# Kernel tuning notes

Hardware: AMD Instinct MI355X
Metric: run time of the kernel (lower is better)

Reference implementation:

```python
import jax, jax.numpy as jnp
import numpy as np

NC = 4
X = Y = Z = 64
IMG_SHAPE = (96, 96, 96)
SPAN = 2          # FILTER_SIZE = [5,5,5]
NUM_ITER = 4
DIL = 2           # DILATION = 2.0
SMOOTH_DISTANCE_INIT = 0.3
PRIOR_DISTANCE_INIT = 0.3


def _ind(d):
    # mirrors _get_ind from the torch code
    return (d, 0) if d > 0 else (0, -d)


def _sl(a, b):
    # slice(a, -b) with -0 -> None, mirrors _negative
    return slice(a, -b if b else None)


def _offsets():
    for dx in range(-SPAN, SPAN + 1):
        for dy in range(-SPAN, SPAN + 1):
            for dz in range(-SPAN, SPAN + 1):
                yield dx, dy, dz


def _lin_resize_axis(x, axis, out):
    # 1D linear interpolation matching torch align_corners=True
    n = x.shape[axis]
    if out == n:
        return x
    pos = jnp.arange(out, dtype=x.dtype) * ((n - 1) / (out - 1))
    i0 = jnp.clip(jnp.floor(pos).astype(jnp.int32), 0, n - 1)
    i1 = jnp.clip(i0 + 1, 0, n - 1)
    w = pos - i0.astype(x.dtype)
    shp = [1] * x.ndim
    shp[axis] = out
    w = w.reshape(shp)
    return jnp.take(x, i0, axis=axis) * (1 - w) + jnp.take(x, i1, axis=axis) * w


def _resize3d(x, out_sz):
    # trilinear, align_corners=True, separable over the 3 spatial axes of [b,c,X,Y,Z]
    for ax, o in zip((2, 3, 4), out_sz):
        x = _lin_resize_axis(x, ax, o)
    return x


def _smooth_gaussian(feats):
    # feats: [b, c, X, Y, Z] -> gaussian [b, 5,5,5, X, Y, Z]
    b = feats.shape[0]
    sp = feats.shape[2:]
    g = jnp.zeros((b, 5, 5, 5) + sp, feats.dtype)
    for dx, dy, dz in _offsets():
        dx1, dx2 = _ind(dx); dy1, dy2 = _ind(dy); dz1, dz2 = _ind(dz)
        a = feats[:, :, _sl(dx1, dx2), _sl(dy1, dy2), _sl(dz1, dz2)]
        c = feats[:, :, _sl(dx2, dx1), _sl(dy2, dy1), _sl(dz2, dz1)]
        e = jnp.exp(-0.5 * jnp.sum((a - c) ** 2, axis=1))
        g = g.at[:, dx + SPAN, dy + SPAN, dz + SPAN,
                 _sl(dx2, dx1), _sl(dy2, dy1), _sl(dz2, dz1)].set(e)
    return g


def _prior_gaussian(f1, f2):
    # f1, f2: [b, c, x, y, z] (already downsampled) -> [b, 5,5,5, x, y, z]
    b = f1.shape[0]
    sp = f1.shape[2:]
    g = jnp.zeros((b, 5, 5, 5) + sp, f1.dtype)
    for dx, dy, dz in _offsets():
        dx1, dx2 = _ind(dx); dy1, dy2 = _ind(dy); dz1, dz2 = _ind(dz)
        a = f1[:, :, _sl(dx2, dx1), _sl(dy2, dy1), _sl(dz2, dz1)]
        c = f2[:, :, _sl(dx1, dx2), _sl(dy1, dy2), _sl(dz1, dz2)]
        e = jnp.exp(-0.5 * jnp.sum((a - c) ** 2, axis=1))
        g = g.at[:, dx + SPAN, dy + SPAN, dz + SPAN,
                 _sl(dx2, dx1), _sl(dy2, dy1), _sl(dz2, dz1)].set(e)
    return g


def _message(p, g):
    # p: [b, nc, x, y, z]; g: [b, 5,5,5, x, y, z]
    out = jnp.zeros_like(p)
    for dx, dy, dz in _offsets():
        dx1, dx2 = _ind(dx); dy1, dy2 = _ind(dy); dz1, dz2 = _ind(dz)
        a = p[:, :, _sl(dx1, dx2), _sl(dy1, dy2), _sl(dz1, dz2)]
        w = g[:, None, dx + SPAN, dy + SPAN, dz + SPAN,
              _sl(dx2, dx1), _sl(dy2, dy1), _sl(dz2, dz1)]
        out = out.at[:, :, _sl(dx2, dx1), _sl(dy2, dy1), _sl(dz2, dz1)].add(a * w)
    return out


def setup_inputs() -> dict:
    key = jax.random.key(0)
    ks = jax.random.split(key, 6)
    unary = jax.random.normal(ks[0], (1, NC, X, Y, Z), jnp.float32)
    img = jax.random.normal(ks[1], (1, 2, X, Y, Z), jnp.float32)
    atlas = jax.random.normal(ks[2], (1, 2, X, Y, Z), jnp.float32)
    atlas_label = jax.random.uniform(ks[3], (1, X, Y, Z, NC), jnp.float32)
    patch_start = jax.random.randint(ks[4], (1, 3), 0, 32, jnp.int32)
    return {
        "unary": unary,
        "img": img,
        "atlas": atlas,
        "atlas_label": atlas_label,
        "patch_start": patch_start,
        "smooth_norm": jnp.array([1.0 / SMOOTH_DISTANCE_INIT], jnp.float32),
        "smooth_weight": jnp.ones((NC,), jnp.float32),
        "prior_norm": jnp.array([1.0 / PRIOR_DISTANCE_INIT], jnp.float32),
        "prior_weight": jnp.ones(IMG_SHAPE, jnp.float32),
        "compat_w": jnp.eye(NC, dtype=jnp.float32),
    }


def reference(unary, img, atlas, atlas_label, patch_start,
              smooth_norm, smooth_weight, prior_norm, prior_weight, compat_w):
    b, nc, x, y, z = unary.shape
    ds = (x // DIL, y // DIL, z // DIL)  # floor(in*0.5) == ceil(in/2) for even dims

    # similarity kernels
    sg = _smooth_gaussian(img * smooth_norm)                      # [b,5,5,5,x,y,z]
    f1 = _resize3d(img * prior_norm, ds)
    f2 = _resize3d(atlas * prior_norm, ds)
    pg = _prior_gaussian(f1, f2)                                  # [b,5,5,5,x/2,y/2,z/2]

    # prior message is independent of q_values: compute once
    al = jnp.transpose(atlas_label, (0, 4, 1, 2, 3))              # [b,nc,x,y,z]
    al_ds = _resize3d(al, ds)
    pm = _resize3d(_message(al_ds, pg), (x, y, z))                # [b,nc,x,y,z]
    pw = jax.lax.dynamic_slice(
        prior_weight,
        (patch_start[0, 0], patch_start[0, 1], patch_start[0, 2]),
        (x, y, z))
    prior_term = pw[None, None] * pm

    q = unary
    for _ in range(NUM_ITER):
        p = jax.nn.softmax(q, axis=1)
        sm = _message(p, sg)
        pred = smooth_weight[None, :, None, None, None] * sm + prior_term
        q = unary + jnp.einsum('oc,bcxyz->boxyz', compat_w, pred)  # 1x1x1 compat conv
    return q
```

## Files before the change

kernel.cpp:

```cpp
#include <hip/hip_runtime.h>

#define NN 64
#define N3 (64*64*64)
#define DS 32
#define DS3 (32*32*32)

#define LOG2E 1.4426950408889634f
#define FSCALE 0.8493218002880191f

typedef _Float16 h2  __attribute__((ext_vector_type(2)));
typedef __fp16   h2f __attribute__((ext_vector_type(2)));

__device__ __forceinline__ float fexp2(float x) { return __builtin_amdgcn_exp2f(x); }

__device__ __forceinline__ h2 u2h(unsigned u) { union { unsigned u; h2 h; } c; c.u = u; return c.h; }
__device__ __forceinline__ unsigned h2u(h2 h) { union { unsigned u; h2 h; } c; c.h = h; return c.u; }
__device__ __forceinline__ h2 pkh(float a, float b) {
    union { h2f a; h2 b; } c; c.a = __builtin_amdgcn_cvt_pkrtz(a, b); return c.b;
}
__device__ __forceinline__ float fdot2(h2 a, h2 b) {
    union { h2 h; h2f f; } ca, cb; ca.h = a; cb.h = b;
    return __builtin_amdgcn_fdot2(ca.f, cb.f, 0.0f, false);
}

__device__ __forceinline__ void axw(int j, float scale, int nmax, int& i0, int& i1, float& w) {
    float pos = (float)j * scale;
    int f = (int)floorf(pos);
    if (f < 0) f = 0;
    if (f > nmax) f = nmax;
    i0 = f;
    i1 = (f + 1 <= nmax) ? f + 1 : nmax;
    w = pos - (float)f;
}


__global__ __launch_bounds__(128) void k_downsample(
    const float* __restrict__ img, const float* __restrict__ atlas,
    const float* __restrict__ alabel, const float* __restrict__ pnorm,
    unsigned* __restrict__ f1pk, uint4* __restrict__ nb)
{
    int idx = blockIdx.x * 128 + threadIdx.x;
    int z = idx & 31, y = (idx >> 5) & 31, x = idx >> 10;

    const float scale = 63.0f / 31.0f;
    int x0,x1,y0,y1,z0,z1; float wx,wy,wz;
    axw(x, scale, 63, x0, x1, wx);
    axw(y, scale, 63, y0, y1, wy);
    axw(z, scale, 63, z0, z1, wz);

    float w000=(1-wx)*(1-wy)*(1-wz), w001=(1-wx)*(1-wy)*wz;
    float w010=(1-wx)*wy*(1-wz),     w011=(1-wx)*wy*wz;
    float w100=wx*(1-wy)*(1-wz),     w101=wx*(1-wy)*wz;
    float w110=wx*wy*(1-wz),         w111=wx*wy*wz;

    int c000=(x0*NN+y0)*NN+z0, c001=(x0*NN+y0)*NN+z1;
    int c010=(x0*NN+y1)*NN+z0, c011=(x0*NN+y1)*NN+z1;
    int c100=(x1*NN+y0)*NN+z0, c101=(x1*NN+y0)*NN+z1;
    int c110=(x1*NN+y1)*NN+z0, c111=(x1*NN+y1)*NN+z1;

    auto tri = [&](const float* p) -> float {
        return p[c000]*w000 + p[c001]*w001 + p[c010]*w010 + p[c011]*w011
             + p[c100]*w100 + p[c101]*w101 + p[c110]*w110 + p[c111]*w111;
    };
    float pnf = pnorm[0] * FSCALE;
    f1pk[idx] = h2u(pkh(pnf*tri(img), pnf*tri(img + N3)));

    auto tril = [&](int c) -> float {
        return alabel[c000*4+c]*w000 + alabel[c001*4+c]*w001 + alabel[c010*4+c]*w010 + alabel[c011*4+c]*w011
             + alabel[c100*4+c]*w100 + alabel[c101*4+c]*w101 + alabel[c110*4+c]*w110 + alabel[c111*4+c]*w111;
    };
    nb[idx] = make_uint4(h2u(pkh(pnf*tri(atlas), pnf*tri(atlas + N3))),
                         h2u(pkh(tril(0), tril(1))),
                         h2u(pkh(tril(2), tril(3))), 0u);
}

__global__ __launch_bounds__(128) void k_prior_msg(
    const unsigned* __restrict__ f1pk, const uint4* __restrict__ nb,
    float4* __restrict__ pm)
{
    int idx = blockIdx.x * 128 + threadIdx.x;
    int z = idx & 31, y = (idx >> 5) & 31, x = idx >> 10;

    h2 ncf = -u2h(f1pk[idx]);
    float a0=0.f, a1=0.f, a2=0.f, a3=0.f;
    for (int dx = -2; dx <= 2; ++dx) {
        int xx = x + dx; if ((unsigned)xx >= DS) continue;
        for (int dy = -2; dy <= 2; ++dy) {
            int yy = y + dy; if ((unsigned)yy >= DS) continue;
            int base = (xx*DS + yy)*DS;
            #pragma unroll
            for (int dz = -2; dz <= 2; ++dz) {
                int zz = z + dz; if ((unsigned)zz >= DS) continue;
                uint4 v = nb[base + zz];
                h2 d = u2h(v.x) + ncf;
                float t = fdot2(d, d);
                float w = fexp2(-t);
                h2 l01 = u2h(v.y), l23 = u2h(v.z);
                a0 += w*(float)l01.x; a1 += w*(float)l01.y;
                a2 += w*(float)l23.x; a3 += w*(float)l23.y;
            }
        }
    }
    pm[idx] = make_float4(a0, a1, a2, a3);
}


#define TXD 8
#define TYD 8
#define TZR 8
#define RZ 2
#define TZD (TZR*RZ)
#define HX 12
#define HY 12
#define HZ 20
#define PZ 22

template<bool QV_IN, bool QV_OUT>
__global__ __launch_bounds__(1024, 4) void k_iter(
    const float* __restrict__ qin,
    const float* __restrict__ unary,
    const float* __restrict__ img,
    const float* __restrict__ snorm,
    const float* __restrict__ sweight,
    const float* __restrict__ compat,
    const float4* __restrict__ pm,
    const float* __restrict__ pweight,
    const int* __restrict__ pstart,
    float* __restrict__ qout)
{
    __shared__ __align__(16) uint2    pS[HX][HY][PZ];
    __shared__ __align__(8)  unsigned fS[HX][HY][PZ];
    __shared__ __align__(16) float4   accS[TXD*TYD*TZR][2];

    const int tzg = threadIdx.x, ty = threadIdx.y;
    const int tx = threadIdx.z & 7, s = threadIdx.z >> 3;
    const int x0b = blockIdx.z * TXD, y0b = blockIdx.y * TYD, z0b = blockIdx.x * TZD;
    const int tid = threadIdx.x + TZR*threadIdx.y + TZR*TYD*threadIdx.z;
    const float sc = snorm[0] * FSCALE;

    #pragma unroll
    for (int rr = 0; rr < 3; ++rr) {
        int i = tid + rr*1024;
        if (i < HX*HY*HZ) {
            int lz = i % HZ; int r = i / HZ;
            int ly = r % HY; int lx = r / HY;
            int gx = x0b + lx - 2, gy = y0b + ly - 2, gz = z0b + lz - 2;
            uint2 pu = make_uint2(0u, 0u);
            unsigned fu = 0u;
            if ((unsigned)gx < NN && (unsigned)gy < NN && (unsigned)gz < NN) {
                int g = (gx*NN + gy)*NN + gz;
                float q0, q1, q2, q3;
                if (QV_IN) {
                    float4 qv = reinterpret_cast<const float4*>(qin)[g];
                    q0 = qv.x; q1 = qv.y; q2 = qv.z; q3 = qv.w;
                } else {
                    q0 = qin[g]; q1 = qin[g+N3]; q2 = qin[g+2*N3]; q3 = qin[g+3*N3];
                }
                float m = fmaxf(fmaxf(q0,q1), fmaxf(q2,q3));
                float e0 = fexp2((q0-m)*LOG2E);
                float e1 = fexp2((q1-m)*LOG2E);
                float e2 = fexp2((q2-m)*LOG2E);
                float e3 = fexp2((q3-m)*LOG2E);
                float inv = 1.0f/(e0+e1+e2+e3);
                pu = make_uint2(h2u(pkh(e0*inv, e1*inv)), h2u(pkh(e2*inv, e3*inv)));
                fu = h2u(pkh(img[g]*sc, img[g+N3]*sc));
            }
            pS[lx][ly][lz] = pu;
            fS[lx][ly][lz] = fu;
        }
    }

    const int tz0 = tzg * RZ;
    const int gx = x0b + tx, gy = y0b + ty, gz = z0b + tz0;

    float4 pr0 = make_float4(0.f,0.f,0.f,0.f), pr1 = make_float4(0.f,0.f,0.f,0.f);
    if (s == 1) {
        const float S13 = 31.0f / 63.0f;
        float posx = (float)gx * S13; int xc0 = (int)posx; float wxf = posx - (float)xc0;
        int xc1 = xc0 < 31 ? xc0+1 : 31;
        float posy = (float)gy * S13; int yc0 = (int)posy; float wyf = posy - (float)yc0;
        int yc1 = yc0 < 31 ? yc0+1 : 31;
        int r00i = (xc0*DS+yc0)*DS, r01i = (xc0*DS+yc1)*DS;
        int r10i = (xc1*DS+yc0)*DS, r11i = (xc1*DS+yc1)*DS;
        auto upz = [&](int gzv) -> float4 {
            float posz = (float)gzv * S13; int zc0 = (int)posz; float wzf = posz - (float)zc0;
            int zc1 = zc0 < 31 ? zc0+1 : 31;
            float4 p000 = pm[r00i+zc0], p001 = pm[r00i+zc1];
            float4 p010 = pm[r01i+zc0], p011 = pm[r01i+zc1];
            float4 p100 = pm[r10i+zc0], p101 = pm[r10i+zc1];
            float4 p110 = pm[r11i+zc0], p111 = pm[r11i+zc1];
            float w000=(1-wxf)*(1-wyf)*(1-wzf), w001=(1-wxf)*(1-wyf)*wzf;
            float w010=(1-wxf)*wyf*(1-wzf),     w011=(1-wxf)*wyf*wzf;
            float w100=wxf*(1-wyf)*(1-wzf),     w101=wxf*(1-wyf)*wzf;
            float w110=wxf*wyf*(1-wzf),         w111=wxf*wyf*wzf;
            float4 r;
            r.x = w000*p000.x + w001*p001.x + w010*p010.x + w011*p011.x + w100*p100.x + w101*p101.x + w110*p110.x + w111*p111.x;
            r.y = w000*p000.y + w001*p001.y + w010*p010.y + w011*p011.y + w100*p100.y + w101*p101.y + w110*p110.y + w111*p111.y;
            r.z = w000*p000.z + w001*p001.z + w010*p010.z + w011*p011.z + w100*p100.z + w101*p101.z + w110*p110.z + w111*p111.z;
            r.w = w000*p000.w + w001*p001.w + w010*p010.w + w011*p011.w + w100*p100.w + w101*p101.w + w110*p110.w + w111*p111.w;
            return r;
        };
        pr0 = upz(gz);
        pr1 = upz(gz+1);
        int ps0 = pstart[0], ps1 = pstart[1], ps2 = pstart[2];
        int pwbase = (ps0+gx)*96*96 + (ps1+gy)*96 + ps2 + gz;
        float pwa = pweight[pwbase], pwb = pweight[pwbase+1];
        pr0.x *= pwa; pr0.y *= pwa; pr0.z *= pwa; pr0.w *= pwa;
        pr1.x *= pwb; pr1.y *= pwb; pr1.z *= pwb; pr1.w *= pwb;
    }

    __syncthreads();

    h2 ncf0 = -u2h(fS[tx+2][ty+2][tz0+2]);
    h2 ncf1 = -u2h(fS[tx+2][ty+2][tz0+3]);

    float4 acc0 = make_float4(0.f,0.f,0.f,0.f);
    float4 acc1 = make_float4(0.f,0.f,0.f,0.f);

    for (int p = s; p < 25; p += 2) {
        int dx = p / 5, dy = p - dx*5;
        const uint4* pp = reinterpret_cast<const uint4*>(&pS[tx+dx][ty+dy][tz0]);
        const uint2* fp = reinterpret_cast<const uint2*>(&fS[tx+dx][ty+dy][tz0]);
        uint4 qa = pp[0], qb = pp[1], qc = pp[2];
        uint2 fa = fp[0], fb = fp[1], fc = fp[2];

        unsigned fz[6]  = { fa.x, fa.y, fb.x, fb.y, fc.x, fc.y };
        unsigned p01[6] = { qa.x, qa.z, qb.x, qb.z, qc.x, qc.z };
        unsigned p23[6] = { qa.y, qa.w, qb.y, qb.w, qc.y, qc.w };

        #pragma unroll
        for (int dz = 0; dz < 5; ++dz) {
            {
                h2 d = u2h(fz[dz]) + ncf0;
                float t = fdot2(d, d);
                float w = fexp2(-t);
                h2 a = u2h(p01[dz]), b = u2h(p23[dz]);
                acc0.x += w*(float)a.x; acc0.y += w*(float)a.y;
                acc0.z += w*(float)b.x; acc0.w += w*(float)b.y;
            }
            {
                h2 d = u2h(fz[dz+1]) + ncf1;
                float t = fdot2(d, d);
                float w = fexp2(-t);
                h2 a = u2h(p01[dz+1]), b = u2h(p23[dz+1]);
                acc1.x += w*(float)a.x; acc1.y += w*(float)a.y;
                acc1.z += w*(float)b.x; acc1.w += w*(float)b.y;
            }
        }
    }

    const int pid = (tx*TYD + ty)*TZR + tzg;
    if (s == 0) {
        accS[pid][0] = acc0;
        accS[pid][1] = acc1;
    }
    __syncthreads();

    if (s == 1) {
        float4 o0 = accS[pid][0], o1 = accS[pid][1];
        acc0.x += o0.x; acc0.y += o0.y; acc0.z += o0.z; acc0.w += o0.w;
        acc1.x += o1.x; acc1.y += o1.y; acc1.z += o1.z; acc1.w += o1.w;

        const int g = (gx*NN + gy)*NN + gz;
        float2 un0 = *(const float2*)(unary + 0*N3 + g);
        float2 un1 = *(const float2*)(unary + 1*N3 + g);
        float2 un2 = *(const float2*)(unary + 2*N3 + g);
        float2 un3 = *(const float2*)(unary + 3*N3 + g);
        float sw0 = sweight[0], sw1 = sweight[1], sw2 = sweight[2], sw3 = sweight[3];
        float cw[16];
        #pragma unroll
        for (int k = 0; k < 16; ++k) cw[k] = compat[k];

        float p0, p1, p2, p3;
        float r00, r10, r20, r30, r01, r11, r21, r31;
        p0 = sw0*acc0.x + pr0.x; p1 = sw1*acc0.y + pr0.y; p2 = sw2*acc0.z + pr0.z; p3 = sw3*acc0.w + pr0.w;
        r00 = un0.x + cw[0]*p0  + cw[1]*p1  + cw[2]*p2  + cw[3]*p3;
        r10 = un1.x + cw[4]*p0  + cw[5]*p1  + cw[6]*p2  + cw[7]*p3;
        r20 = un2.x + cw[8]*p0  + cw[9]*p1  + cw[10]*p2 + cw[11]*p3;
        r30 = un3.x + cw[12]*p0 + cw[13]*p1 + cw[14]*p2 + cw[15]*p3;
        p0 = sw0*acc1.x + pr1.x; p1 = sw1*acc1.y + pr1.y; p2 = sw2*acc1.z + pr1.z; p3 = sw3*acc1.w + pr1.w;
        r01 = un0.y + cw[0]*p0  + cw[1]*p1  + cw[2]*p2  + cw[3]*p3;
        r11 = un1.y + cw[4]*p0  + cw[5]*p1  + cw[6]*p2  + cw[7]*p3;
        r21 = un2.y + cw[8]*p0  + cw[9]*p1  + cw[10]*p2 + cw[11]*p3;
        r31 = un3.y + cw[12]*p0 + cw[13]*p1 + cw[14]*p2 + cw[15]*p3;

        if (QV_OUT) {
            reinterpret_cast<float4*>(qout)[g]   = make_float4(r00, r10, r20, r30);
            reinterpret_cast<float4*>(qout)[g+1] = make_float4(r01, r11, r21, r31);
        } else {
            *(float2*)(qout + 0*N3 + g) = make_float2(r00, r01);
            *(float2*)(qout + 1*N3 + g) = make_float2(r10, r11);
            *(float2*)(qout + 2*N3 + g) = make_float2(r20, r21);
            *(float2*)(qout + 3*N3 + g) = make_float2(r30, r31);
        }
    }
}


extern "C" void kernel_launch(void* const* d_in, const int* in_sizes, int n_in,
                              void* d_out, int out_size, void* d_ws, size_t ws_size,
                              hipStream_t stream)
{
    const float* unary   = (const float*)d_in[0];
    const float* img     = (const float*)d_in[1];
    const float* atlas   = (const float*)d_in[2];
    const float* alabel  = (const float*)d_in[3];
    const int*   pstart  = (const int*)d_in[4];
    const float* snorm   = (const float*)d_in[5];
    const float* sweight = (const float*)d_in[6];
    const float* pnorm   = (const float*)d_in[7];
    const float* pweight = (const float*)d_in[8];
    const float* compat  = (const float*)d_in[9];
    float* out = (float*)d_out;
    float* ws  = (float*)d_ws;

    float*    qA   = ws;
    float*    qB   = ws + 4*N3;
    unsigned* f1pk = (unsigned*)(ws + 8*N3);
    uint4*    nbuf = (uint4*)(f1pk + DS3);
    float4*   pm   = (float4*)(nbuf + DS3);

    k_downsample<<<DS3/128, 128, 0, stream>>>(img, atlas, alabel, pnorm, f1pk, nbuf);
    k_prior_msg<<<DS3/128, 128, 0, stream>>>(f1pk, nbuf, pm);

    dim3 grid(NN/TZD, NN/TYD, NN/TXD), block(TZR, TYD, 16);
    k_iter<false,true><<<grid, block, 0, stream>>>(unary, unary, img, snorm, sweight, compat, pm, pweight, pstart, qA);
    k_iter<true, true><<<grid, block, 0, stream>>>(qA,    unary, img, snorm, sweight, compat, pm, pweight, pstart, qB);
    k_iter<true, true><<<grid, block, 0, stream>>>(qB,    unary, img, snorm, sweight, compat, pm, pweight, pstart, qA);
    k_iter<true,false><<<grid, block, 0, stream>>>(qA,    unary, img, snorm, sweight, compat, pm, pweight, pstart, out);
}
```

Measured before the change: 95.58 us.

## Fuse four mean-field iterations into one cooperative kernel with grid sync

Replaces four separate per-iteration launches with a single cooperative launch that loops over the iterations and uses grid-wide syncs between them. The image feature tile, the prior upsample term and the centre features are loaded once and kept in shared memory and registers across iterations, removing launch gaps and repeated loads. The message accumulation also moves from fp32 scalar FMAs to packed fp16 FMAs, which cuts instruction count but lowers accumulation precision. Grid sync needs every block resident at once (the grid is 256 blocks of 1024 threads) and adds its own barrier cost.

```diff
diff --git a/kernel.cpp b/kernel.cpp
--- a/kernel.cpp
+++ b/kernel.cpp
@@ -1,4 +1,7 @@
 #include <hip/hip_runtime.h>
+#include <hip/hip_cooperative_groups.h>
+
+namespace cg = cooperative_groups;
 
 #define NN 64
 #define N3 (64*64*64)
@@ -115,9 +118,7 @@
 #define HZ 20
 #define PZ 22
 
-template<bool QV_IN, bool QV_OUT>
-__global__ __launch_bounds__(1024, 4) void k_iter(
-    const float* __restrict__ qin,
+__global__ __launch_bounds__(1024) void k_coop(
     const float* __restrict__ unary,
     const float* __restrict__ img,
     const float* __restrict__ snorm,
@@ -126,11 +127,15 @@
     const float4* __restrict__ pm,
     const float* __restrict__ pweight,
     const int* __restrict__ pstart,
-    float* __restrict__ qout)
+    float* __restrict__ qA,
+    float* __restrict__ qB,
+    float* __restrict__ out)
 {
     __shared__ __align__(16) uint2    pS[HX][HY][PZ];
     __shared__ __align__(8)  unsigned fS[HX][HY][PZ];
-    __shared__ __align__(16) float4   accS[TXD*TYD*TZR][2];
+    __shared__ __align__(16) uint2    accS[TXD*TYD*TZR][2];
+
+    cg::grid_group gridg = cg::this_grid();
 
     const int tzg = threadIdx.x, ty = threadIdx.y;
     const int tx = threadIdx.z & 7, s = threadIdx.z >> 3;
@@ -145,33 +150,19 @@
             int lz = i % HZ; int r = i / HZ;
             int ly = r % HY; int lx = r / HY;
             int gx = x0b + lx - 2, gy = y0b + ly - 2, gz = z0b + lz - 2;
-            uint2 pu = make_uint2(0u, 0u);
             unsigned fu = 0u;
             if ((unsigned)gx < NN && (unsigned)gy < NN && (unsigned)gz < NN) {
                 int g = (gx*NN + gy)*NN + gz;
-                float q0, q1, q2, q3;
-                if (QV_IN) {
-                    float4 qv = reinterpret_cast<const float4*>(qin)[g];
-                    q0 = qv.x; q1 = qv.y; q2 = qv.z; q3 = qv.w;
-                } else {
-                    q0 = qin[g]; q1 = qin[g+N3]; q2 = qin[g+2*N3]; q3 = qin[g+3*N3];
-                }
-                float m = fmaxf(fmaxf(q0,q1), fmaxf(q2,q3));
-                float e0 = fexp2((q0-m)*LOG2E);
-                float e1 = fexp2((q1-m)*LOG2E);
-                float e2 = fexp2((q2-m)*LOG2E);
-                float e3 = fexp2((q3-m)*LOG2E);
-                float inv = 1.0f/(e0+e1+e2+e3);
-                pu = make_uint2(h2u(pkh(e0*inv, e1*inv)), h2u(pkh(e2*inv, e3*inv)));
                 fu = h2u(pkh(img[g]*sc, img[g+N3]*sc));
             }
-            pS[lx][ly][lz] = pu;
             fS[lx][ly][lz] = fu;
         }
     }
 
     const int tz0 = tzg * RZ;
     const int gx = x0b + tx, gy = y0b + ty, gz = z0b + tz0;
+    const int g = (gx*NN + gy)*NN + gz;
+    const int pid = (tx*TYD + ty)*TZR + tzg;
 
     float4 pr0 = make_float4(0.f,0.f,0.f,0.f), pr1 = make_float4(0.f,0.f,0.f,0.f);
     if (s == 1) {
@@ -211,88 +202,124 @@
 
     __syncthreads();
 
-    h2 ncf0 = -u2h(fS[tx+2][ty+2][tz0+2]);
-    h2 ncf1 = -u2h(fS[tx+2][ty+2][tz0+3]);
-
-    float4 acc0 = make_float4(0.f,0.f,0.f,0.f);
-    float4 acc1 = make_float4(0.f,0.f,0.f,0.f);
-
-    for (int p = s; p < 25; p += 2) {
-        int dx = p / 5, dy = p - dx*5;
-        const uint4* pp = reinterpret_cast<const uint4*>(&pS[tx+dx][ty+dy][tz0]);
-        const uint2* fp = reinterpret_cast<const uint2*>(&fS[tx+dx][ty+dy][tz0]);
-        uint4 qa = pp[0], qb = pp[1], qc = pp[2];
-        uint2 fa = fp[0], fb = fp[1], fc = fp[2];
-
-        unsigned fz[6]  = { fa.x, fa.y, fb.x, fb.y, fc.x, fc.y };
-        unsigned p01[6] = { qa.x, qa.z, qb.x, qb.z, qc.x, qc.z };
-        unsigned p23[6] = { qa.y, qa.w, qb.y, qb.w, qc.y, qc.w };
+    const h2 ncf0 = -u2h(fS[tx+2][ty+2][tz0+2]);
+    const h2 ncf1 = -u2h(fS[tx+2][ty+2][tz0+3]);
+
+    for (int it = 0; it < 4; ++it) {
+        const float* qin  = (it == 0) ? unary : ((it == 2) ? qB : qA);
+        float*       qout = (it == 0) ? qA : ((it == 1) ? qB : ((it == 2) ? qA : out));
+        const bool vec_in  = (it != 0);
+        const bool vec_out = (it != 3);
 
         #pragma unroll
-        for (int dz = 0; dz < 5; ++dz) {
-            {
-                h2 d = u2h(fz[dz]) + ncf0;
-                float t = fdot2(d, d);
-                float w = fexp2(-t);
-                h2 a = u2h(p01[dz]), b = u2h(p23[dz]);
-                acc0.x += w*(float)a.x; acc0.y += w*(float)a.y;
-                acc0.z += w*(float)b.x; acc0.w += w*(float)b.y;
-            }
-            {
-                h2 d = u2h(fz[dz+1]) + ncf1;
-                float t = fdot2(d, d);
-                float w = fexp2(-t);
-                h2 a = u2h(p01[dz+1]), b = u2h(p23[dz+1]);
-                acc1.x += w*(float)a.x; acc1.y += w*(float)a.y;
-                acc1.z += w*(float)b.x; acc1.w += w*(float)b.y;
-            }
-        }
-    }
-
-    const int pid = (tx*TYD + ty)*TZR + tzg;
-    if (s == 0) {
-        accS[pid][0] = acc0;
-        accS[pid][1] = acc1;
-    }
-    __syncthreads();
-
-    if (s == 1) {
-        float4 o0 = accS[pid][0], o1 = accS[pid][1];
-        acc0.x += o0.x; acc0.y += o0.y; acc0.z += o0.z; acc0.w += o0.w;
-        acc1.x += o1.x; acc1.y += o1.y; acc1.z += o1.z; acc1.w += o1.w;
-
-        const int g = (gx*NN + gy)*NN + gz;
-        float2 un0 = *(const float2*)(unary + 0*N3 + g);
-        float2 un1 = *(const float2*)(unary + 1*N3 + g);
-        float2 un2 = *(const float2*)(unary + 2*N3 + g);
-        float2 un3 = *(const float2*)(unary + 3*N3 + g);
-        float sw0 = sweight[0], sw1 = sweight[1], sw2 = sweight[2], sw3 = sweight[3];
-        float cw[16];
-        #pragma unroll
-        for (int k = 0; k < 16; ++k) cw[k] = compat[k];
-
-        float p0, p1, p2, p3;
-        float r00, r10, r20, r30, r01, r11, r21, r31;
-        p0 = sw0*acc0.x + pr0.x; p1 = sw1*acc0.y + pr0.y; p2 = sw2*acc0.z + pr0.z; p3 = sw3*acc0.w + pr0.w;
-        r00 = un0.x + cw[0]*p0  + cw[1]*p1  + cw[2]*p2  + cw[3]*p3;
-        r10 = un1.x + cw[4]*p0  + cw[5]*p1  + cw[6]*p2  + cw[7]*p3;
-        r20 = un2.x + cw[8]*p0  + cw[9]*p1  + cw[10]*p2 + cw[11]*p3;
-        r30 = un3.x + cw[12]*p0 + cw[13]*p1 + cw[14]*p2 + cw[15]*p3;
-        p0 = sw0*acc1.x + pr1.x; p1 = sw1*acc1.y + pr1.y; p2 = sw2*acc1.z + pr1.z; p3 = sw3*acc1.w + pr1.w;
-        r01 = un0.y + cw[0]*p0  + cw[1]*p1  + cw[2]*p2  + cw[3]*p3;
-        r11 = un1.y + cw[4]*p0  + cw[5]*p1  + cw[6]*p2  + cw[7]*p3;
-        r21 = un2.y + cw[8]*p0  + cw[9]*p1  + cw[10]*p2 + cw[11]*p3;
-        r31 = un3.y + cw[12]*p0 + cw[13]*p1 + cw[14]*p2 + cw[15]*p3;
-
-        if (QV_OUT) {
-            reinterpret_cast<float4*>(qout)[g]   = make_float4(r00, r10, r20, r30);
-            reinterpret_cast<float4*>(qout)[g+1] = make_float4(r01, r11, r21, r31);
-        } else {
-            *(float2*)(qout + 0*N3 + g) = make_float2(r00, r01);
-            *(float2*)(qout + 1*N3 + g) = make_float2(r10, r11);
-            *(float2*)(qout + 2*N3 + g) = make_float2(r20, r21);
-            *(float2*)(qout + 3*N3 + g) = make_float2(r30, r31);
-        }
+        for (int rr = 0; rr < 3; ++rr) {
+            int i = tid + rr*1024;
+            if (i < HX*HY*HZ) {
+                int lz = i % HZ; int r = i / HZ;
+                int ly = r % HY; int lx = r / HY;
+                int ggx = x0b + lx - 2, ggy = y0b + ly - 2, ggz = z0b + lz - 2;
+                uint2 pu = make_uint2(0u, 0u);
+                if ((unsigned)ggx < NN && (unsigned)ggy < NN && (unsigned)ggz < NN) {
+                    int gg = (ggx*NN + ggy)*NN + ggz;
+                    float q0, q1, q2, q3;
+                    if (vec_in) {
+                        float4 qv = reinterpret_cast<const float4*>(qin)[gg];
+                        q0 = qv.x; q1 = qv.y; q2 = qv.z; q3 = qv.w;
+                    } else {
+                        q0 = qin[gg]; q1 = qin[gg+N3]; q2 = qin[gg+2*N3]; q3 = qin[gg+3*N3];
+                    }
+                    float m = fmaxf(fmaxf(q0,q1), fmaxf(q2,q3));
+                    float e0 = fexp2((q0-m)*LOG2E);
+                    float e1 = fexp2((q1-m)*LOG2E);
+                    float e2 = fexp2((q2-m)*LOG2E);
+                    float e3 = fexp2((q3-m)*LOG2E);
+                    float inv = 1.0f/(e0+e1+e2+e3);
+                    pu = make_uint2(h2u(pkh(e0*inv, e1*inv)), h2u(pkh(e2*inv, e3*inv)));
+                }
+                pS[lx][ly][lz] = pu;
+            }
+        }
+        __syncthreads();
+
+        h2 a01_0 = (h2)0, a23_0 = (h2)0, a01_1 = (h2)0, a23_1 = (h2)0;
+
+        for (int p = s; p < 25; p += 2) {
+            int dx = p / 5, dy = p - dx*5;
+            const uint4* pp = reinterpret_cast<const uint4*>(&pS[tx+dx][ty+dy][tz0]);
+            const uint2* fp = reinterpret_cast<const uint2*>(&fS[tx+dx][ty+dy][tz0]);
+            uint4 qa = pp[0], qb = pp[1], qc = pp[2];
+            uint2 fa = fp[0], fb = fp[1], fc = fp[2];
+
+            unsigned fz[6]  = { fa.x, fa.y, fb.x, fb.y, fc.x, fc.y };
+            unsigned p01[6] = { qa.x, qa.z, qb.x, qb.z, qc.x, qc.z };
+            unsigned p23[6] = { qa.y, qa.w, qb.y, qb.w, qc.y, qc.w };
+
+            #pragma unroll
+            for (int dz = 0; dz < 5; ++dz) {
+                {
+                    h2 d = u2h(fz[dz]) + ncf0;
+                    float w = fexp2(-fdot2(d, d));
+                    h2 w2 = pkh(w, w);
+                    a01_0 = w2 * u2h(p01[dz]) + a01_0;
+                    a23_0 = w2 * u2h(p23[dz]) + a23_0;
+                }
+                {
+                    h2 d = u2h(fz[dz+1]) + ncf1;
+                    float w = fexp2(-fdot2(d, d));
+                    h2 w2 = pkh(w, w);
+                    a01_1 = w2 * u2h(p01[dz+1]) + a01_1;
+                    a23_1 = w2 * u2h(p23[dz+1]) + a23_1;
+                }
+            }
+        }
+
+        if (s == 0) {
+            accS[pid][0] = make_uint2(h2u(a01_0), h2u(a23_0));
+            accS[pid][1] = make_uint2(h2u(a01_1), h2u(a23_1));
+        }
+        __syncthreads();
+
+        if (s == 1) {
+            uint2 o0 = accS[pid][0], o1 = accS[pid][1];
+            h2 t01_0 = a01_0 + u2h(o0.x), t23_0 = a23_0 + u2h(o0.y);
+            h2 t01_1 = a01_1 + u2h(o1.x), t23_1 = a23_1 + u2h(o1.y);
+
+            float2 un0 = *(const float2*)(unary + 0*N3 + g);
+            float2 un1 = *(const float2*)(unary + 1*N3 + g);
+            float2 un2 = *(const float2*)(unary + 2*N3 + g);
+            float2 un3 = *(const float2*)(unary + 3*N3 + g);
+            float sw0 = sweight[0], sw1 = sweight[1], sw2 = sweight[2], sw3 = sweight[3];
+            float cw[16];
+            #pragma unroll
+            for (int k = 0; k < 16; ++k) cw[k] = compat[k];
+
+            float p0, p1, p2, p3;
+            float r00, r10, r20, r30, r01, r11, r21, r31;
+            p0 = sw0*(float)t01_0.x + pr0.x; p1 = sw1*(float)t01_0.y + pr0.y;
+            p2 = sw2*(float)t23_0.x + pr0.z; p3 = sw3*(float)t23_0.y + pr0.w;
+            r00 = un0.x + cw[0]*p0  + cw[1]*p1  + cw[2]*p2  + cw[3]*p3;
+            r10 = un1.x + cw[4]*p0  + cw[5]*p1  + cw[6]*p2  + cw[7]*p3;
+            r20 = un2.x + cw[8]*p0  + cw[9]*p1  + cw[10]*p2 + cw[11]*p3;
+            r30 = un3.x + cw[12]*p0 + cw[13]*p1 + cw[14]*p2 + cw[15]*p3;
+            p0 = sw0*(float)t01_1.x + pr1.x; p1 = sw1*(float)t01_1.y + pr1.y;
+            p2 = sw2*(float)t23_1.x + pr1.z; p3 = sw3*(float)t23_1.y + pr1.w;
+            r01 = un0.y + cw[0]*p0  + cw[1]*p1  + cw[2]*p2  + cw[3]*p3;
+            r11 = un1.y + cw[4]*p0  + cw[5]*p1  + cw[6]*p2  + cw[7]*p3;
+            r21 = un2.y + cw[8]*p0  + cw[9]*p1  + cw[10]*p2 + cw[11]*p3;
+            r31 = un3.y + cw[12]*p0 + cw[13]*p1 + cw[14]*p2 + cw[15]*p3;
+
+            if (vec_out) {
+                reinterpret_cast<float4*>(qout)[g]   = make_float4(r00, r10, r20, r30);
+                reinterpret_cast<float4*>(qout)[g+1] = make_float4(r01, r11, r21, r31);
+            } else {
+                *(float2*)(qout + 0*N3 + g) = make_float2(r00, r01);
+                *(float2*)(qout + 1*N3 + g) = make_float2(r10, r11);
+                *(float2*)(qout + 2*N3 + g) = make_float2(r20, r21);
+                *(float2*)(qout + 3*N3 + g) = make_float2(r30, r31);
+            }
+        }
+
+        if (it != 3) gridg.sync();
     }
 }
 
@@ -324,8 +351,9 @@
     k_prior_msg<<<DS3/128, 128, 0, stream>>>(f1pk, nbuf, pm);
 
     dim3 grid(NN/TZD, NN/TYD, NN/TXD), block(TZR, TYD, 16);
-    k_iter<false,true><<<grid, block, 0, stream>>>(unary, unary, img, snorm, sweight, compat, pm, pweight, pstart, qA);
-    k_iter<true, true><<<grid, block, 0, stream>>>(qA,    unary, img, snorm, sweight, compat, pm, pweight, pstart, qB);
-    k_iter<true, true><<<grid, block, 0, stream>>>(qB,    unary, img, snorm, sweight, compat, pm, pweight, pstart, qA);
-    k_iter<true,false><<<grid, block, 0, stream>>>(qA,    unary, img, snorm, sweight, compat, pm, pweight, pstart, out);
-}
+    void* args[] = {
+        (void*)&unary, (void*)&img, (void*)&snorm, (void*)&sweight, (void*)&compat,
+        (void*)&pm, (void*)&pweight, (void*)&pstart, (void*)&qA, (void*)&qB, (void*)&out
+    };
+    hipLaunchCooperativeKernel((const void*)k_coop, grid, block, args, 0, stream);
+}
```

After: 204.2 us. 114% more time.

## Split stencil taps four ways per voxel with packed half accumulation

Applied to the files above, without the earlier changes.

The main iteration kernel now uses smaller z tiles (8 instead of 16) and splits the 25 dx/dy taps across four thread groups instead of two, so each block covers fewer voxels with more threads per voxel. Accumulation switches from fp32 scalar FMAs to packed fp16 FMAs, and partial sums are reduced through shared memory as packed halves. The prior-term upsample moves to the group that does the final reduction and overlaps with the stencil work. This raises parallelism and shortens the ALU chain, at the cost of a larger halo-to-interior ratio and lower fp16 accumulation precision.

```diff
diff --git a/kernel.cpp b/kernel.cpp
--- a/kernel.cpp
+++ b/kernel.cpp
@@ -107,16 +107,16 @@
 
 #define TXD 8
 #define TYD 8
-#define TZR 8
+#define TZD 8
+#define TZR 4
 #define RZ 2
-#define TZD (TZR*RZ)
 #define HX 12
 #define HY 12
-#define HZ 20
-#define PZ 22
+#define HZ 12
+#define PZ 14
 
 template<bool QV_IN, bool QV_OUT>
-__global__ __launch_bounds__(1024, 4) void k_iter(
+__global__ __launch_bounds__(1024, 8) void k_iter(
     const float* __restrict__ qin,
     const float* __restrict__ unary,
     const float* __restrict__ img,
@@ -130,16 +130,16 @@
 {
     __shared__ __align__(16) uint2    pS[HX][HY][PZ];
     __shared__ __align__(8)  unsigned fS[HX][HY][PZ];
-    __shared__ __align__(16) float4   accS[TXD*TYD*TZR][2];
+    __shared__ __align__(16) uint4    accS[3][TXD*TYD*TZR];
 
     const int tzg = threadIdx.x, ty = threadIdx.y;
     const int tx = threadIdx.z & 7, s = threadIdx.z >> 3;
     const int x0b = blockIdx.z * TXD, y0b = blockIdx.y * TYD, z0b = blockIdx.x * TZD;
-    const int tid = threadIdx.x + TZR*threadIdx.y + TZR*TYD*threadIdx.z;
+    const int tid = threadIdx.x + TZR*threadIdx.y + (TZR*TYD)*threadIdx.z;
     const float sc = snorm[0] * FSCALE;
 
     #pragma unroll
-    for (int rr = 0; rr < 3; ++rr) {
+    for (int rr = 0; rr < 2; ++rr) {
         int i = tid + rr*1024;
         if (i < HX*HY*HZ) {
             int lz = i % HZ; int r = i / HZ;
@@ -169,12 +169,57 @@
             fS[lx][ly][lz] = fu;
         }
     }
+    __syncthreads();
 
     const int tz0 = tzg * RZ;
     const int gx = x0b + tx, gy = y0b + ty, gz = z0b + tz0;
 
+    const h2 ncf0 = -u2h(fS[tx+2][ty+2][tz0+2]);
+    const h2 ncf1 = -u2h(fS[tx+2][ty+2][tz0+3]);
+
+    h2 a01_0 = (h2)0, a23_0 = (h2)0, a01_1 = (h2)0, a23_1 = (h2)0;
+
+    #pragma unroll
+    for (int pp = 0; pp < 7; ++pp) {
+        int p = (3 - s) + 4*pp;
+        if (p < 25) {
+            int dx = p / 5, dy = p - 5*dx;
+            const uint4* pv = reinterpret_cast<const uint4*>(&pS[tx+dx][ty+dy][tz0]);
+            const uint2* fv = reinterpret_cast<const uint2*>(&fS[tx+dx][ty+dy][tz0]);
+            uint4 qa = pv[0], qb = pv[1], qc = pv[2];
+            uint2 fa = fv[0], fb = fv[1], fc = fv[2];
+
+            unsigned fz[6]  = { fa.x, fa.y, fb.x, fb.y, fc.x, fc.y };
+            unsigned p01[6] = { qa.x, qa.z, qb.x, qb.z, qc.x, qc.z };
+            unsigned p23[6] = { qa.y, qa.w, qb.y, qb.w, qc.y, qc.w };
+
+            #pragma unroll
+            for (int dz = 0; dz < 5; ++dz) {
+                {
+                    h2 d = u2h(fz[dz]) + ncf0;
+                    float w = fexp2(-fdot2(d, d));
+                    h2 w2 = pkh(w, w);
+                    a01_0 = w2 * u2h(p01[dz]) + a01_0;
+                    a23_0 = w2 * u2h(p23[dz]) + a23_0;
+                }
+                {
+                    h2 d = u2h(fz[dz+1]) + ncf1;
+                    float w = fexp2(-fdot2(d, d));
+                    h2 w2 = pkh(w, w);
+                    a01_1 = w2 * u2h(p01[dz+1]) + a01_1;
+                    a23_1 = w2 * u2h(p23[dz+1]) + a23_1;
+                }
+            }
+        }
+    }
+
+    const int pid = (tx*TYD + ty)*TZR + tzg;
+    if (s != 0) {
+        accS[s-1][pid] = make_uint4(h2u(a01_0), h2u(a23_0), h2u(a01_1), h2u(a23_1));
+    }
+
     float4 pr0 = make_float4(0.f,0.f,0.f,0.f), pr1 = make_float4(0.f,0.f,0.f,0.f);
-    if (s == 1) {
+    if (s == 0) {
         const float S13 = 31.0f / 63.0f;
         float posx = (float)gx * S13; int xc0 = (int)posx; float wxf = posx - (float)xc0;
         int xc1 = xc0 < 31 ? xc0+1 : 31;
@@ -211,55 +256,13 @@
 
     __syncthreads();
 
-    h2 ncf0 = -u2h(fS[tx+2][ty+2][tz0+2]);
-    h2 ncf1 = -u2h(fS[tx+2][ty+2][tz0+3]);
-
-    float4 acc0 = make_float4(0.f,0.f,0.f,0.f);
-    float4 acc1 = make_float4(0.f,0.f,0.f,0.f);
-
-    for (int p = s; p < 25; p += 2) {
-        int dx = p / 5, dy = p - dx*5;
-        const uint4* pp = reinterpret_cast<const uint4*>(&pS[tx+dx][ty+dy][tz0]);
-        const uint2* fp = reinterpret_cast<const uint2*>(&fS[tx+dx][ty+dy][tz0]);
-        uint4 qa = pp[0], qb = pp[1], qc = pp[2];
-        uint2 fa = fp[0], fb = fp[1], fc = fp[2];
-
-        unsigned fz[6]  = { fa.x, fa.y, fb.x, fb.y, fc.x, fc.y };
-        unsigned p01[6] = { qa.x, qa.z, qb.x, qb.z, qc.x, qc.z };
-        unsigned p23[6] = { qa.y, qa.w, qb.y, qb.w, qc.y, qc.w };
-
+    if (s == 0) {
         #pragma unroll
-        for (int dz = 0; dz < 5; ++dz) {
-            {
-                h2 d = u2h(fz[dz]) + ncf0;
-                float t = fdot2(d, d);
-                float w = fexp2(-t);
-                h2 a = u2h(p01[dz]), b = u2h(p23[dz]);
-                acc0.x += w*(float)a.x; acc0.y += w*(float)a.y;
-                acc0.z += w*(float)b.x; acc0.w += w*(float)b.y;
-            }
-            {
-                h2 d = u2h(fz[dz+1]) + ncf1;
-                float t = fdot2(d, d);
-                float w = fexp2(-t);
-                h2 a = u2h(p01[dz+1]), b = u2h(p23[dz+1]);
-                acc1.x += w*(float)a.x; acc1.y += w*(float)a.y;
-                acc1.z += w*(float)b.x; acc1.w += w*(float)b.y;
-            }
-        }
-    }
-
-    const int pid = (tx*TYD + ty)*TZR + tzg;
-    if (s == 0) {
-        accS[pid][0] = acc0;
-        accS[pid][1] = acc1;
-    }
-    __syncthreads();
-
-    if (s == 1) {
-        float4 o0 = accS[pid][0], o1 = accS[pid][1];
-        acc0.x += o0.x; acc0.y += o0.y; acc0.z += o0.z; acc0.w += o0.w;
-        acc1.x += o1.x; acc1.y += o1.y; acc1.z += o1.z; acc1.w += o1.w;
+        for (int j = 0; j < 3; ++j) {
+            uint4 v = accS[j][pid];
+            a01_0 += u2h(v.x); a23_0 += u2h(v.y);
+            a01_1 += u2h(v.z); a23_1 += u2h(v.w);
+        }
 
         const int g = (gx*NN + gy)*NN + gz;
         float2 un0 = *(const float2*)(unary + 0*N3 + g);
@@ -273,12 +276,14 @@
 
         float p0, p1, p2, p3;
         float r00, r10, r20, r30, r01, r11, r21, r31;
-        p0 = sw0*acc0.x + pr0.x; p1 = sw1*acc0.y + pr0.y; p2 = sw2*acc0.z + pr0.z; p3 = sw3*acc0.w + pr0.w;
+        p0 = sw0*(float)a01_0.x + pr0.x; p1 = sw1*(float)a01_0.y + pr0.y;
+        p2 = sw2*(float)a23_0.x + pr0.z; p3 = sw3*(float)a23_0.y + pr0.w;
         r00 = un0.x + cw[0]*p0  + cw[1]*p1  + cw[2]*p2  + cw[3]*p3;
         r10 = un1.x + cw[4]*p0  + cw[5]*p1  + cw[6]*p2  + cw[7]*p3;
         r20 = un2.x + cw[8]*p0  + cw[9]*p1  + cw[10]*p2 + cw[11]*p3;
         r30 = un3.x + cw[12]*p0 + cw[13]*p1 + cw[14]*p2 + cw[15]*p3;
-        p0 = sw0*acc1.x + pr1.x; p1 = sw1*acc1.y + pr1.y; p2 = sw2*acc1.z + pr1.z; p3 = sw3*acc1.w + pr1.w;
+        p0 = sw0*(float)a01_1.x + pr1.x; p1 = sw1*(float)a01_1.y + pr1.y;
+        p2 = sw2*(float)a23_1.x + pr1.z; p3 = sw3*(float)a23_1.y + pr1.w;
         r01 = un0.y + cw[0]*p0  + cw[1]*p1  + cw[2]*p2  + cw[3]*p3;
         r11 = un1.y + cw[4]*p0  + cw[5]*p1  + cw[6]*p2  + cw[7]*p3;
         r21 = un2.y + cw[8]*p0  + cw[9]*p1  + cw[10]*p2 + cw[11]*p3;
@@ -323,7 +328,7 @@
     k_downsample<<<DS3/128, 128, 0, stream>>>(img, atlas, alabel, pnorm, f1pk, nbuf);
     k_prior_msg<<<DS3/128, 128, 0, stream>>>(f1pk, nbuf, pm);
 
-    dim3 grid(NN/TZD, NN/TYD, NN/TXD), block(TZR, TYD, 16);
+    dim3 grid(NN/TZD, NN/TYD, NN/TXD), block(TZR, TYD, 32);
     k_iter<false,true><<<grid, block, 0, stream>>>(unary, unary, img, snorm, sweight, compat, pm, pweight, pstart, qA);
     k_iter<true, true><<<grid, block, 0, stream>>>(qA,    unary, img, snorm, sweight, compat, pm, pweight, pstart, qB);
     k_iter<true, true><<<grid, block, 0, stream>>>(qB,    unary, img, snorm, sweight, compat, pm, pweight, pstart, qA);
```

Result: faster. 90.31 us (-5.5%).
